# Optimization experiments

Hardware: AMD Instinct MI355X
Metric: run time of the kernel (lower is better)

## Reference

```python
import jax, jax.numpy as jnp
import numpy as np


def _gru(x, w_ih, w_hh, b_ih, b_hh, reverse=False):
    # PyTorch GRU cell math. x: (N, T, Din) -> (N, T, Hh)
    N, T, _ = x.shape
    Hh = w_hh.shape[1]
    xp = jnp.einsum('ntd,gd->ntg', x, w_ih) + b_ih  # (N, T, 3*Hh), input gates precomputed

    def step(h, xp_t):
        gh = h @ w_hh.T + b_hh
        ir, iz, inn = jnp.split(xp_t, 3, axis=-1)
        hr, hz, hn = jnp.split(gh, 3, axis=-1)
        r = jax.nn.sigmoid(ir + hr)
        z = jax.nn.sigmoid(iz + hz)
        n = jnp.tanh(inn + r * hn)
        h_new = (1.0 - z) * n + z * h
        return h_new, h_new

    h0 = jnp.zeros((N, Hh), x.dtype)
    _, ys = jax.lax.scan(step, h0, jnp.swapaxes(xp, 0, 1), reverse=reverse)
    return jnp.swapaxes(ys, 0, 1)


def _bigru(x, pf, pb):
    return jnp.concatenate([_gru(x, *pf), _gru(x, *pb, reverse=True)], axis=-1)


def _attn(out, w, b, ctx):
    # out: (N, T, H). tanh(Linear) -> context dot -> softmax -> weighted sum
    u = jnp.tanh(jnp.einsum('nth,gh->ntg', out, w) + b)
    a = jax.nn.softmax(u @ ctx, axis=-1)  # (N, T)
    return jnp.einsum('nt,nth->nh', a, out)


def setup_inputs() -> dict:
    key = jax.random.key(0)
    H, Hh = 512, 256
    S, B, Nsent = 2048, 16, 16
    L = S // Nsent
    ks = jax.random.split(key, 32)

    def p(k, shape):
        return jax.random.normal(k, shape, jnp.float32) * 0.05

    starts = jnp.arange(Nsent, dtype=jnp.int32) * L
    spans = jnp.stack([starts, starts + L], axis=-1)  # (Nsent, 2)
    spans = jnp.broadcast_to(spans, (B, Nsent, 2))

    inp = {
        'token_feats': jax.random.normal(ks[0], (S, B, H), jnp.float32),
        'sentence_spans': spans,
        # word BiGRU params (forward / backward directions)
        'w_wih_f': p(ks[1], (3 * Hh, H)), 'w_whh_f': p(ks[2], (3 * Hh, Hh)),
        'w_bih_f': p(ks[3], (3 * Hh,)), 'w_bhh_f': p(ks[4], (3 * Hh,)),
        'w_wih_b': p(ks[5], (3 * Hh, H)), 'w_whh_b': p(ks[6], (3 * Hh, Hh)),
        'w_bih_b': p(ks[7], (3 * Hh,)), 'w_bhh_b': p(ks[8], (3 * Hh,)),
        # sentence BiGRU params
        's_wih_f': p(ks[9], (3 * Hh, H)), 's_whh_f': p(ks[10], (3 * Hh, Hh)),
        's_bih_f': p(ks[11], (3 * Hh,)), 's_bhh_f': p(ks[12], (3 * Hh,)),
        's_wih_b': p(ks[13], (3 * Hh, H)), 's_whh_b': p(ks[14], (3 * Hh, Hh)),
        's_bih_b': p(ks[15], (3 * Hh,)), 's_bhh_b': p(ks[16], (3 * Hh,)),
        # attention params
        'w_attn_w': p(ks[17], (H, H)), 'w_attn_b': p(ks[18], (H,)),
        'w_ctx': jax.random.normal(ks[19], (H,), jnp.float32),
        's_attn_w': p(ks[20], (H, H)), 's_attn_b': p(ks[21], (H,)),
        's_ctx': jax.random.normal(ks[22], (H,), jnp.float32),
    }
    return inp


def reference(token_feats, sentence_spans,
              w_wih_f, w_whh_f, w_bih_f, w_bhh_f,
              w_wih_b, w_whh_b, w_bih_b, w_bhh_b,
              s_wih_f, s_whh_f, s_bih_f, s_bhh_f,
              s_wih_b, s_whh_b, s_bih_b, s_bhh_b,
              w_attn_w, w_attn_b, w_ctx,
              s_attn_w, s_attn_b, s_ctx):
    S, B, H = token_feats.shape
    Nsent = sentence_spans.shape[1]
    L = S // Nsent  # uniform spans: segment b,i = tokens [i*L, (i+1)*L)

    x = jnp.swapaxes(token_feats, 0, 1)  # (B, S, H)
    segs = x.reshape(B * Nsent, L, H)    # all sentences batched together

    # word-level BiGRU + word attention -> sentence vectors
    out_w = _bigru(segs, (w_wih_f, w_whh_f, w_bih_f, w_bhh_f),
                   (w_wih_b, w_whh_b, w_bih_b, w_bhh_b))  # (B*Nsent, L, H)
    sent_vecs = _attn(out_w, w_attn_w, w_attn_b, w_ctx).reshape(B, Nsent, H)

    # sentence-level BiGRU + sentence attention (no padding: all masks true)
    out_s = _bigru(sent_vecs, (s_wih_f, s_whh_f, s_bih_f, s_bhh_f),
                   (s_wih_b, s_whh_b, s_bih_b, s_bhh_b))  # (B, Nsent, H)
    Yh = _attn(out_s, s_attn_w, s_attn_b, s_ctx)  # (B, H)
    return Yh
```

## Files before the change

kernel.cpp:

```cpp
#include <hip/hip_runtime.h>
#include <stdint.h>


using uint32  = unsigned int;
using bf16x8  = __attribute__((ext_vector_type(8))) __bf16;
using floatx4 = __attribute__((ext_vector_type(4))) float;

__device__ __forceinline__ float b2f(unsigned short u) {
    union { uint32 i; float f; } v; v.i = ((uint32)u) << 16; return v.f;
}
__device__ __forceinline__ unsigned short f2b(float f) {
    union { float f; uint32 i; } v; v.f = f;
    uint32 r = v.i + 0x7fffu + ((v.i >> 16) & 1u);
    return (unsigned short)(r >> 16);
}
__device__ __forceinline__ float sigmoidf_(float x) { return 1.f / (1.f + __expf(-x)); }
__device__ __forceinline__ float tanhf_(float x) {
    x = fminf(15.f, fmaxf(-15.f, x));
    float e = __expf(2.f * x);
    return (e - 1.f) / (e + 1.f);
}

__device__ __forceinline__ void gl16(const unsigned short* g, unsigned short* l) {
    __builtin_amdgcn_global_load_lds(
        (const __attribute__((address_space(1))) uint32*)g,
        (__attribute__((address_space(3))) uint32*)l, 16, 0, 0);
}

__device__ __forceinline__ void bar_lgkm() {
    asm volatile("s_waitcnt lgkmcnt(0)");
    __builtin_amdgcn_sched_barrier(0);
    __builtin_amdgcn_s_barrier();
    __builtin_amdgcn_sched_barrier(0);
}

#define O_XPC     0L
#define O_OWHI    50331648L
#define O_OWLO    83886080L
#define O_STATE   117440512L
#define O_SCW     117964800L
#define O_W0HI    118095872L
#define O_W0LO    118882304L
#define O_W1HI    119668736L
#define O_W1LO    120455168L
#define O_WAHI    121241600L
#define O_WALO    121765888L
#define O_S0HI    122290176L
#define O_S0LO    123076608L
#define O_S1HI    123863040L
#define O_S1LO    124649472L
#define O_SAHI    125435904L
#define O_SALO    125960192L
#define O_HW0     126484480L
#define O_HW1     126877696L
#define O_HS0     127270912L
#define O_HS1     127664128L
#define O_SENTHI  128057344L
#define O_SENTLO  128319488L
#define O_XPS     128581632L
#define O_SSTATE  130154496L
#define O_OSHI    130187264L
#define O_OSLO    130449408L
#define O_SCS     130711552L
#define O_TKWH    130712576L
#define O_TKWL    164267008L

__global__ __launch_bounds__(256)
void cvt_hilo6(const float* __restrict__ s0, const float* __restrict__ s1,
               const float* __restrict__ s2, const float* __restrict__ s3,
               const float* __restrict__ s4, const float* __restrict__ s5,
               char* __restrict__ ws)
{
    const int b = blockIdx.x;
    const float* src; unsigned short *hi, *lo; int base;
    if (b < 192)      { src = s0; hi = (unsigned short*)(ws + O_W0HI); lo = (unsigned short*)(ws + O_W0LO); base = b; }
    else if (b < 384) { src = s1; hi = (unsigned short*)(ws + O_W1HI); lo = (unsigned short*)(ws + O_W1LO); base = b - 192; }
    else if (b < 576) { src = s2; hi = (unsigned short*)(ws + O_S0HI); lo = (unsigned short*)(ws + O_S0LO); base = b - 384; }
    else if (b < 768) { src = s3; hi = (unsigned short*)(ws + O_S1HI); lo = (unsigned short*)(ws + O_S1LO); base = b - 576; }
    else if (b < 896) { src = s4; hi = (unsigned short*)(ws + O_WAHI); lo = (unsigned short*)(ws + O_WALO); base = b - 768; }
    else              { src = s5; hi = (unsigned short*)(ws + O_SAHI); lo = (unsigned short*)(ws + O_SALO); base = b - 896; }
    const int idx = (base * 256 + threadIdx.x) * 8;
    float f[8];
    *reinterpret_cast<float4*>(&f[0]) = *reinterpret_cast<const float4*>(src + idx);
    *reinterpret_cast<float4*>(&f[4]) = *reinterpret_cast<const float4*>(src + idx + 4);
    unsigned short h[8], l[8];
    #pragma unroll
    for (int j = 0; j < 8; ++j) {
        h[j] = f2b(f[j]);
        l[j] = f2b(f[j] - b2f(h[j]));
    }
    *reinterpret_cast<uint4*>(hi + idx) = *reinterpret_cast<const uint4*>(h);
    *reinterpret_cast<uint4*>(lo + idx) = *reinterpret_cast<const uint4*>(l);
}

__global__ __launch_bounds__(256)
void cvt_b4(const float* __restrict__ s0, const float* __restrict__ s1,
            const float* __restrict__ s2, const float* __restrict__ s3,
            char* __restrict__ ws)
{
    const int b = blockIdx.x;
    const float* src; unsigned short* dst; int base;
    if (b < 96)       { src = s0; dst = (unsigned short*)(ws + O_HW0); base = b; }
    else if (b < 192) { src = s1; dst = (unsigned short*)(ws + O_HW1); base = b - 96; }
    else if (b < 288) { src = s2; dst = (unsigned short*)(ws + O_HS0); base = b - 192; }
    else              { src = s3; dst = (unsigned short*)(ws + O_HS1); base = b - 288; }
    const int idx = (base * 256 + threadIdx.x) * 8;
    float f[8];
    *reinterpret_cast<float4*>(&f[0]) = *reinterpret_cast<const float4*>(src + idx);
    *reinterpret_cast<float4*>(&f[4]) = *reinterpret_cast<const float4*>(src + idx + 4);
    unsigned short o[8];
    #pragma unroll
    for (int j = 0; j < 8; ++j) o[j] = f2b(f[j]);
    *reinterpret_cast<uint4*>(dst + idx) = *reinterpret_cast<const uint4*>(o);
}

__global__ __launch_bounds__(256)
void cvt_tokfull(const float* __restrict__ tok, unsigned short* __restrict__ whi,
                 unsigned short* __restrict__ wlo)
{
    const int u = blockIdx.x * 256 + threadIdx.x;
    const int h8 = u & 63;
    const int rest = u >> 6;
    const int t = rest & 127, seq = rest >> 7;
    const int sent = seq & 15, b = seq >> 4;
    const long src = ((long)(sent * 128 + t) * 16 + b) * 512 + h8 * 8;
    float f[8];
    *reinterpret_cast<float4*>(&f[0]) = *reinterpret_cast<const float4*>(tok + src);
    *reinterpret_cast<float4*>(&f[4]) = *reinterpret_cast<const float4*>(tok + src + 4);
    unsigned short h[8], l[8];
    #pragma unroll
    for (int j = 0; j < 8; ++j) {
        h[j] = f2b(f[j]);
        l[j] = f2b(f[j] - b2f(h[j]));
    }
    const long dst = (long)rest * 512 + h8 * 8;
    *reinterpret_cast<uint4*>(whi + dst) = *reinterpret_cast<const uint4*>(h);
    *reinterpret_cast<uint4*>(wlo + dst) = *reinterpret_cast<const uint4*>(l);
}

template<int AMODE>
__device__ __forceinline__ long amap(int m, int t0, int sgn) {
    if (AMODE == 1) {
        const int sq = m >> 5, tl = m & 31;
        return (long)(sq * 128 + t0 + sgn * tl) * 512;
    } else if (AMODE == 3) {
        const int n = m >> 4, tl = m & 15;
        return (long)(n * 16 + t0 + sgn * tl) * 512;
    }
    return (long)m * 512;
}

template<int AMODE, int OUT>
__global__ __launch_bounds__(512, 2)
void gemm_t(const unsigned short* __restrict__ Ahi, const unsigned short* __restrict__ Alo,
            const unsigned short* __restrict__ Wh0, const unsigned short* __restrict__ Wl0,
            const unsigned short* __restrict__ Wh1, const unsigned short* __restrict__ Wl1,
            const float* __restrict__ b0, const float* __restrict__ b1,
            float* __restrict__ C, int ldC, long c1off,
            float* __restrict__ score, const float* __restrict__ ctx,
            int t00, int t01, int nbyHalf)
{
    __shared__ __align__(16) unsigned short smem[2 * 32768];

    int bx = blockIdx.x, by = blockIdx.y;
    {
        const int nbx = gridDim.x, nby = gridDim.y;
        if ((nby & 7) == 0) {
            const int l = by * nbx + bx;
            const int xcd = l & 7;
            const int s = l >> 3;
            bx = s % nbx;
            by = xcd * (nby >> 3) + s / nbx;
        }
    }

    const int tid  = threadIdx.x;
    const int lane = tid & 63;
    const int wave = tid >> 6;
    const int wm = wave >> 2, wn = wave & 3;
    const int n_base = bx * 256;
    const int q = lane >> 4;
    const int r = lane & 15;

    const unsigned short* Whi = Wh0;
    const unsigned short* Wlo = Wl0;
    const float* bias = b0;
    float* Cb = C;
    int t0 = t00, sgn = 1, m_base;
    if (nbyHalf > 0 && by >= nbyHalf) {
        Whi = Wh1; Wlo = Wl1; bias = b1; Cb = C + c1off;
        t0 = t01; sgn = -1;
        m_base = (by - nbyHalf) * 256;
    } else {
        m_base = by * 256;
    }

    long aoff[2], woff[2];
    #pragma unroll
    for (int i = 0; i < 2; ++i) {
        const int s = tid + 512 * i;
        const int R = s >> 2, kg = s & 3;
        const int kq = (kg - (R >> 1)) & 3;
        aoff[i] = amap<AMODE>(m_base + R, t0, sgn) + kq * 8;
        woff[i] = (long)(n_base + R) * 512 + kq * 8;
    }

    floatx4 acc[8][4];
    #pragma unroll
    for (int mt = 0; mt < 8; ++mt)
        #pragma unroll
        for (int nt = 0; nt < 4; ++nt) acc[mt][nt] = (floatx4){0.f, 0.f, 0.f, 0.f};

    auto stage = [&](int ts) {
        const int k0 = ts * 32;
        unsigned short* B = smem + (ts & 1) * 32768;
        #pragma unroll
        for (int i = 0; i < 2; ++i) {
            const int ld = (tid + 512 * i) * 8;
            gl16(Ahi + aoff[i] + k0, B + ld);
            gl16(Alo + aoff[i] + k0, B + 8192 + ld);
            gl16(Whi + woff[i] + k0, B + 16384 + ld);
            gl16(Wlo + woff[i] + k0, B + 24576 + ld);
        }
    };

    stage(0);
    asm volatile("s_waitcnt vmcnt(0)");
    __builtin_amdgcn_sched_barrier(0);
    __builtin_amdgcn_s_barrier();
    __builtin_amdgcn_sched_barrier(0);

    for (int t = 0; t < 16; ++t) {
        if (t + 1 < 16) stage(t + 1);

        const unsigned short* B   = smem + (t & 1) * 32768;
        const unsigned short* BAl = B + 8192;
        const unsigned short* BW  = B + 16384;
        const unsigned short* BWl = B + 24576;

        bf16x8 wh[4], wl[4], ah[8], al[8];
        #pragma unroll
        for (int nt = 0; nt < 4; ++nt) {
            const int Rn = wn * 64 + nt * 16 + r;
            const int sn = Rn * 4 + ((q + (Rn >> 1)) & 3);
            wh[nt] = *reinterpret_cast<const bf16x8*>(BW  + sn * 8);
            wl[nt] = *reinterpret_cast<const bf16x8*>(BWl + sn * 8);
        }
        #pragma unroll
        for (int mt = 0; mt < 8; ++mt) {
            const int R = wm * 128 + mt * 16 + r;
            const int s = R * 4 + ((q + (R >> 1)) & 3);
            ah[mt] = *reinterpret_cast<const bf16x8*>(B   + s * 8);
            al[mt] = *reinterpret_cast<const bf16x8*>(BAl + s * 8);
        }
        asm volatile("s_waitcnt lgkmcnt(0)");
        __builtin_amdgcn_sched_barrier(0);

        #pragma unroll
        for (int mt = 0; mt < 8; ++mt)
            #pragma unroll
            for (int nt = 0; nt < 4; ++nt) {
                acc[mt][nt] = __builtin_amdgcn_mfma_f32_16x16x32_bf16(ah[mt], wh[nt], acc[mt][nt], 0, 0, 0);
                acc[mt][nt] = __builtin_amdgcn_mfma_f32_16x16x32_bf16(ah[mt], wl[nt], acc[mt][nt], 0, 0, 0);
                acc[mt][nt] = __builtin_amdgcn_mfma_f32_16x16x32_bf16(al[mt], wh[nt], acc[mt][nt], 0, 0, 0);
            }

        __builtin_amdgcn_sched_barrier(0);
        asm volatile("s_waitcnt vmcnt(0)");
        __builtin_amdgcn_sched_barrier(0);
        __builtin_amdgcn_s_barrier();
        __builtin_amdgcn_sched_barrier(0);
    }

    if (OUT == 0) {
        #pragma unroll
        for (int nt = 0; nt < 4; ++nt) {
            const int n = n_base + wn * 64 + nt * 16 + r;
            const float bs = bias[n];
            #pragma unroll
            for (int mt = 0; mt < 8; ++mt) {
                const int m = m_base + wm * 128 + mt * 16 + q * 4;
                #pragma unroll
                for (int e = 0; e < 4; ++e)
                    Cb[(long)(m + e) * ldC + n] = acc[mt][nt][e] + bs;
            }
        }
    } else {
        #pragma unroll
        for (int mt = 0; mt < 8; ++mt) {
            float p[4] = {0.f, 0.f, 0.f, 0.f};
            #pragma unroll
            for (int nt = 0; nt < 4; ++nt) {
                const int n = n_base + wn * 64 + nt * 16 + r;
                const float cx = ctx[n];
                const float bs = bias[n];
                #pragma unroll
                for (int e = 0; e < 4; ++e)
                    p[e] += cx * tanhf_(acc[mt][nt][e] + bs);
            }
            #pragma unroll
            for (int mk = 1; mk < 16; mk <<= 1) {
                #pragma unroll
                for (int e = 0; e < 4; ++e) p[e] += __shfl_xor(p[e], mk, 64);
            }
            if (r == 0) {
                const int m = m_base + wm * 128 + mt * 16 + q * 4;
                #pragma unroll
                for (int e = 0; e < 4; ++e)
                    atomicAdd(&score[m + e], p[e]);
            }
        }
    }
}

template<int AMODE, int OUT>
__global__ __launch_bounds__(256)
void gemm_d(const unsigned short* __restrict__ Ahi, const unsigned short* __restrict__ Alo,
            const unsigned short* __restrict__ Wh0, const unsigned short* __restrict__ Wl0,
            const unsigned short* __restrict__ Wh1, const unsigned short* __restrict__ Wl1,
            const float* __restrict__ b0, const float* __restrict__ b1,
            float* __restrict__ C, int ldC, long c1off,
            float* __restrict__ score, const float* __restrict__ ctx,
            int t00, int t01, int nbyHalf)
{
    __shared__ __align__(16) unsigned short smem[2 * 16384];

    int bx = blockIdx.x, by = blockIdx.y;
    {
        const int nbx = gridDim.x, nby = gridDim.y;
        if ((nby & 7) == 0) {
            const int l = by * nbx + bx;
            const int xcd = l & 7;
            const int s = l >> 3;
            bx = s % nbx;
            by = xcd * (nby >> 3) + s / nbx;
        }
    }

    const int tid  = threadIdx.x;
    const int lane = tid & 63;
    const int wave = tid >> 6;
    const int wm = wave >> 1, wn = wave & 1;
    const int n_base = bx * 128;
    const int q = lane >> 4;
    const int r = lane & 15;

    const unsigned short* Whi = Wh0;
    const unsigned short* Wlo = Wl0;
    const float* bias = b0;
    float* Cb = C;
    int t0 = t00, sgn = 1, m_base;
    if (nbyHalf > 0 && by >= nbyHalf) {
        Whi = Wh1; Wlo = Wl1; bias = b1; Cb = C + c1off;
        t0 = t01; sgn = -1;
        m_base = (by - nbyHalf) * 128;
    } else {
        m_base = by * 128;
    }

    long aoff[2], woff[2];
    #pragma unroll
    for (int i = 0; i < 2; ++i) {
        const int s = tid + 256 * i;
        const int R = s >> 2, kg = s & 3;
        const int kq = (kg - (R >> 1)) & 3;
        aoff[i] = amap<AMODE>(m_base + R, t0, sgn) + kq * 8;
        woff[i] = (long)(n_base + R) * 512 + kq * 8;
    }

    floatx4 acc[4][4];
    #pragma unroll
    for (int mt = 0; mt < 4; ++mt)
        #pragma unroll
        for (int nt = 0; nt < 4; ++nt) acc[mt][nt] = (floatx4){0.f, 0.f, 0.f, 0.f};

    auto stage = [&](int ts) {
        const int k0 = ts * 32;
        unsigned short* B = smem + (ts & 1) * 16384;
        #pragma unroll
        for (int i = 0; i < 2; ++i) {
            const int ld = (tid + 256 * i) * 8;
            gl16(Ahi + aoff[i] + k0, B + ld);
            gl16(Alo + aoff[i] + k0, B + 4096 + ld);
            gl16(Whi + woff[i] + k0, B + 8192 + ld);
            gl16(Wlo + woff[i] + k0, B + 12288 + ld);
        }
    };

    stage(0);
    for (int t = 0; t < 16; ++t) {
        stage(t + 1 < 16 ? t + 1 : 15);
        asm volatile("s_waitcnt vmcnt(8)\n\ts_barrier" ::: "memory");

        const unsigned short* B = smem + (t & 1) * 16384;
        bf16x8 ah[4], al[4];
        #pragma unroll
        for (int mt = 0; mt < 4; ++mt) {
            const int R = wm * 64 + mt * 16 + r;
            const int s = R * 4 + ((q + (R >> 1)) & 3);
            ah[mt] = *reinterpret_cast<const bf16x8*>(B + s * 8);
            al[mt] = *reinterpret_cast<const bf16x8*>(B + 4096 + s * 8);
        }
        #pragma unroll
        for (int nt = 0; nt < 4; ++nt) {
            const int Rn = wn * 64 + nt * 16 + r;
            const int sn = Rn * 4 + ((q + (Rn >> 1)) & 3);
            bf16x8 wh = *reinterpret_cast<const bf16x8*>(B + 8192 + sn * 8);
            bf16x8 wl = *reinterpret_cast<const bf16x8*>(B + 12288 + sn * 8);
            #pragma unroll
            for (int mt = 0; mt < 4; ++mt) {
                acc[mt][nt] = __builtin_amdgcn_mfma_f32_16x16x32_bf16(ah[mt], wh, acc[mt][nt], 0, 0, 0);
                acc[mt][nt] = __builtin_amdgcn_mfma_f32_16x16x32_bf16(ah[mt], wl, acc[mt][nt], 0, 0, 0);
                acc[mt][nt] = __builtin_amdgcn_mfma_f32_16x16x32_bf16(al[mt], wh, acc[mt][nt], 0, 0, 0);
            }
        }
        asm volatile("s_waitcnt lgkmcnt(0)\n\ts_barrier" ::: "memory");
    }
    asm volatile("s_waitcnt vmcnt(0)" ::: "memory");

    if (OUT == 0) {
        #pragma unroll
        for (int nt = 0; nt < 4; ++nt) {
            const int n = n_base + wn * 64 + nt * 16 + r;
            const float bs = bias[n];
            #pragma unroll
            for (int mt = 0; mt < 4; ++mt) {
                const int m = m_base + wm * 64 + mt * 16 + q * 4;
                #pragma unroll
                for (int e = 0; e < 4; ++e)
                    Cb[(long)(m + e) * ldC + n] = acc[mt][nt][e] + bs;
            }
        }
    } else {
        #pragma unroll
        for (int mt = 0; mt < 4; ++mt) {
            float p[4] = {0.f, 0.f, 0.f, 0.f};
            #pragma unroll
            for (int nt = 0; nt < 4; ++nt) {
                const int n = n_base + wn * 64 + nt * 16 + r;
                const float cx = ctx[n];
                const float bs = bias[n];
                #pragma unroll
                for (int e = 0; e < 4; ++e)
                    p[e] += cx * tanhf_(acc[mt][nt][e] + bs);
            }
            #pragma unroll
            for (int mk = 1; mk < 16; mk <<= 1) {
                #pragma unroll
                for (int e = 0; e < 4; ++e) p[e] += __shfl_xor(p[e], mk, 64);
            }
            if (r == 0) {
                const int m = m_base + wm * 64 + mt * 16 + q * 4;
                #pragma unroll
                for (int e = 0; e < 4; ++e)
                    atomicAdd(&score[m + e], p[e]);
            }
        }
    }
}

__global__ __launch_bounds__(512, 2)
void gru2(const float* __restrict__ xp,
          const unsigned short* __restrict__ Wf,
          const unsigned short* __restrict__ Wb,
          const float* __restrict__ bhf, const float* __restrict__ bhb,
          float* __restrict__ state,
          unsigned short* __restrict__ ohi, unsigned short* __restrict__ olo,
          int steps, int t0f, int t0b, int groups, int Tout)
{
    __shared__ float preS[8][6][16][4];
    __shared__ unsigned short Bf[2][4096];

    const int tid  = threadIdx.x;
    const int lane = tid & 63;
    const int w    = tid >> 6;
    const int dir  = blockIdx.x / groups;
    const int g    = blockIdx.x % groups;
    const int nseq = groups * 2;
    const unsigned short* W = dir ? Wb : Wf;
    const float* bh = dir ? bhb : bhf;
    const int t0  = dir ? t0b : t0f;
    const int sgn = dir ? -1 : 1;

    const int s  = lane & 1;
    const int lr = lane >> 1;
    const int u  = w * 32 + lr;

    const float bhr = bh[u], bhz = bh[u + 256], bhn = bh[u + 512];

    bf16x8 wf[6][8];
    {
        const int rl = lane & 15;
        const int kf = (lane >> 4) * 8;
        #pragma unroll
        for (int mt = 0; mt < 6; ++mt) {
            const int R = (mt >> 1) * 256 + w * 32 + (mt & 1) * 16 + rl;
            #pragma unroll
            for (int kk = 0; kk < 8; ++kk)
                wf[mt][kk] = *reinterpret_cast<const bf16x8*>(
                    W + (long)R * 256 + kk * 32 + kf);
        }
    }

    #pragma unroll
    for (int i = 0; i < 8; ++i)
        reinterpret_cast<uint32*>(Bf)[tid * 8 + i] = 0;

    float h = state[((long)dir * nseq + g * 2 + s) * 256 + u];
    const int bposHi = (w * 64 + (lr >> 3) * 16 + s) * 8 + (lr & 7);
    const int bposLo = (w * 64 + (lr >> 3) * 16 + 2 + s) * 8 + (lr & 7);
    {
        const unsigned short hb = f2b(h);
        Bf[0][bposHi] = hb;
        Bf[0][bposLo] = f2b(h - b2f(hb));
    }
    bar_lgkm();

    const float* xbase = xp + (long)dir * nseq * steps * 768
                       + (long)(g * 2 + s) * steps * 768;

    float xr = xbase[u], xz = xbase[256 + u], xn = xbase[512 + u];

    const int c  = lane & 15;
    const int q  = lane >> 4;
    const int rit  = lr & 15;
    const int hsel = lr >> 4;

    for (int st = 0; st < steps; ++st) {
        const int t = t0 + sgn * st;
        const int cur = st & 1;

        const int sn2 = (st + 1 < steps) ? st + 1 : st;
        const float* xb = xbase + (long)sn2 * 768;
        const float nxr = xb[u];
        const float nxz = xb[256 + u];
        const float nxn = xb[512 + u];

        floatx4 acc[6];
        #pragma unroll
        for (int mt = 0; mt < 6; ++mt) acc[mt] = (floatx4){0.f, 0.f, 0.f, 0.f};
        #pragma unroll
        for (int kk = 0; kk < 8; ++kk) {
            bf16x8 bv = *reinterpret_cast<const bf16x8*>(&Bf[cur][(kk * 64 + lane) * 8]);
            #pragma unroll
            for (int mt = 0; mt < 6; ++mt)
                acc[mt] = __builtin_amdgcn_mfma_f32_16x16x32_bf16(wf[mt][kk], bv, acc[mt], 0, 0, 0);
        }

        if (c < 4) {
            #pragma unroll
            for (int mt = 0; mt < 6; ++mt)
                #pragma unroll
                for (int e = 0; e < 4; ++e)
                    preS[w][mt][q * 4 + e][c] = acc[mt][e];
        }
        asm volatile("s_waitcnt lgkmcnt(0)");
        __builtin_amdgcn_sched_barrier(0);

        {
            const float4 fr = *reinterpret_cast<const float4*>(&preS[w][0 + hsel][rit][0]);
            const float4 fz = *reinterpret_cast<const float4*>(&preS[w][2 + hsel][rit][0]);
            const float4 fn = *reinterpret_cast<const float4*>(&preS[w][4 + hsel][rit][0]);
            const float pr = (s ? fr.y : fr.x) + (s ? fr.w : fr.z);
            const float pz = (s ? fz.y : fz.x) + (s ? fz.w : fz.z);
            const float pn = (s ? fn.y : fn.x) + (s ? fn.w : fn.z);
            const float rg = sigmoidf_(xr + pr + bhr);
            const float zg = sigmoidf_(xz + pz + bhz);
            const float nn = tanhf_(xn + rg * (pn + bhn));
            h = (1.f - zg) * nn + zg * h;
            const unsigned short hb = f2b(h);
            const unsigned short lb = f2b(h - b2f(hb));
            Bf[cur ^ 1][bposHi] = hb;
            Bf[cur ^ 1][bposLo] = lb;
            const long orow = ((long)(g * 2 + s) * Tout + t) * 512 + dir * 256 + u;
            ohi[orow] = hb;
            olo[orow] = lb;
        }
        xr = nxr; xz = nxz; xn = nxn;
        bar_lgkm();
    }

    state[((long)dir * nseq + g * 2 + s) * 256 + u] = h;
}

template<int MODE, int T>
__global__ __launch_bounds__(256)
void attn_wsum(const float* __restrict__ score,
               const unsigned short* __restrict__ fhi,
               const unsigned short* __restrict__ flo,
               void* __restrict__ o1, void* __restrict__ o2)
{
    const int n = blockIdx.x;
    const int tid = threadIdx.x;
    __shared__ float a[T];
    __shared__ float e[T];
    if (tid < T) a[tid] = score[n * T + tid];
    __syncthreads();
    float mx = -1e30f;
    #pragma unroll
    for (int t = 0; t < T; ++t) mx = fmaxf(mx, a[t]);
    if (tid < T) e[tid] = __expf(a[tid] - mx);
    __syncthreads();
    float sm = 0.f;
    #pragma unroll
    for (int t = 0; t < T; ++t) sm += e[t];
    const float inv = 1.f / sm;
    float acc0 = 0.f, acc1 = 0.f;
    #pragma unroll 8
    for (int t = 0; t < T; ++t) {
        const float w = e[t] * inv;
        const long base = ((long)n * T + t) * 512;
        acc0 += w * (b2f(fhi[base + tid])       + b2f(flo[base + tid]));
        acc1 += w * (b2f(fhi[base + tid + 256]) + b2f(flo[base + tid + 256]));
    }
    if (MODE == 1) {
        float* o = (float*)o1;
        o[n * 512 + tid] = acc0;
        o[n * 512 + tid + 256] = acc1;
    } else {
        unsigned short* oh = (unsigned short*)o1;
        unsigned short* ol = (unsigned short*)o2;
        const unsigned short h0 = f2b(acc0), h1 = f2b(acc1);
        oh[n * 512 + tid]       = h0;  ol[n * 512 + tid]       = f2b(acc0 - b2f(h0));
        oh[n * 512 + tid + 256] = h1;  ol[n * 512 + tid + 256] = f2b(acc1 - b2f(h1));
    }
}

extern "C" void kernel_launch(void* const* d_in, const int* in_sizes, int n_in,
                              void* d_out, int out_size, void* d_ws, size_t ws_size,
                              hipStream_t stream) {
    const float* tok      = (const float*)d_in[0];
    const float* w_wih_f  = (const float*)d_in[2];
    const float* w_whh_f  = (const float*)d_in[3];
    const float* w_bih_f  = (const float*)d_in[4];
    const float* w_bhh_f  = (const float*)d_in[5];
    const float* w_wih_b  = (const float*)d_in[6];
    const float* w_whh_b  = (const float*)d_in[7];
    const float* w_bih_b  = (const float*)d_in[8];
    const float* w_bhh_b  = (const float*)d_in[9];
    const float* s_wih_f  = (const float*)d_in[10];
    const float* s_whh_f  = (const float*)d_in[11];
    const float* s_bih_f  = (const float*)d_in[12];
    const float* s_bhh_f  = (const float*)d_in[13];
    const float* s_wih_b  = (const float*)d_in[14];
    const float* s_whh_b  = (const float*)d_in[15];
    const float* s_bih_b  = (const float*)d_in[16];
    const float* s_bhh_b  = (const float*)d_in[17];
    const float* w_attn_b = (const float*)d_in[19];
    const float* w_ctx    = (const float*)d_in[20];
    const float* s_attn_b = (const float*)d_in[22];
    const float* s_ctx    = (const float*)d_in[23];

    char* ws = (char*)d_ws;
    float*          xpc   = (float*)(ws + O_XPC);
    unsigned short* owhi  = (unsigned short*)(ws + O_OWHI);
    unsigned short* owlo  = (unsigned short*)(ws + O_OWLO);
    float*          state = (float*)(ws + O_STATE);
    float*          score_w = (float*)(ws + O_SCW);
    unsigned short* W0HI  = (unsigned short*)(ws + O_W0HI);
    unsigned short* W0LO  = (unsigned short*)(ws + O_W0LO);
    unsigned short* W1HI  = (unsigned short*)(ws + O_W1HI);
    unsigned short* W1LO  = (unsigned short*)(ws + O_W1LO);
    unsigned short* WAHI  = (unsigned short*)(ws + O_WAHI);
    unsigned short* WALO  = (unsigned short*)(ws + O_WALO);
    unsigned short* S0HI  = (unsigned short*)(ws + O_S0HI);
    unsigned short* S0LO  = (unsigned short*)(ws + O_S0LO);
    unsigned short* S1HI  = (unsigned short*)(ws + O_S1HI);
    unsigned short* S1LO  = (unsigned short*)(ws + O_S1LO);
    unsigned short* SAHI  = (unsigned short*)(ws + O_SAHI);
    unsigned short* SALO  = (unsigned short*)(ws + O_SALO);
    unsigned short* HW0   = (unsigned short*)(ws + O_HW0);
    unsigned short* HW1   = (unsigned short*)(ws + O_HW1);
    unsigned short* HS0   = (unsigned short*)(ws + O_HS0);
    unsigned short* HS1   = (unsigned short*)(ws + O_HS1);
    unsigned short* senthi = (unsigned short*)(ws + O_SENTHI);
    unsigned short* sentlo = (unsigned short*)(ws + O_SENTLO);
    float*          xp_s  = (float*)(ws + O_XPS);
    float*          sstate = (float*)(ws + O_SSTATE);
    unsigned short* oshi  = (unsigned short*)(ws + O_OSHI);
    unsigned short* oslo  = (unsigned short*)(ws + O_OSLO);
    float*          score_s = (float*)(ws + O_SCS);
    unsigned short* tkwh  = (unsigned short*)(ws + O_TKWH);
    unsigned short* tkwl  = (unsigned short*)(ws + O_TKWL);

    const dim3 blk(256);

    hipMemsetAsync(ws + O_STATE,  0, 524288, stream);
    hipMemsetAsync(ws + O_SSTATE, 0, 32768, stream);
    hipMemsetAsync(ws + O_SCW,    0, 131072, stream);
    hipMemsetAsync(ws + O_SCS,    0, 1024, stream);

    cvt_hilo6<<<dim3(1024), blk, 0, stream>>>(w_wih_f, w_wih_b, s_wih_f, s_wih_b,
                                              (const float*)d_in[18], (const float*)d_in[21], ws);
    cvt_b4<<<dim3(384), blk, 0, stream>>>(w_whh_f, w_whh_b, s_whh_f, s_whh_b, ws);
    cvt_tokfull<<<dim3(8192), blk, 0, stream>>>(tok, tkwh, tkwl);

    const long XDW = 256L * 32 * 768;
    for (int c = 0; c < 4; ++c) {
        gemm_t<1, 0><<<dim3(3, 64), dim3(512), 0, stream>>>(
            tkwh, tkwl, W0HI, W0LO, W1HI, W1LO, w_bih_f, w_bih_b,
            xpc, 768, XDW, nullptr, nullptr, 32 * c, 127 - 32 * c, 32);
        gru2<<<dim3(256), dim3(512), 0, stream>>>(
            xpc, HW0, HW1, w_bhh_f, w_bhh_b, state, owhi, owlo,
            32, 32 * c, 127 - 32 * c, 128, 128);
    }

    gemm_t<2, 1><<<dim3(2, 128), dim3(512), 0, stream>>>(
        owhi, owlo, WAHI, WALO, WAHI, WALO, w_attn_b, w_attn_b,
        nullptr, 0, 0, score_w, w_ctx, 0, 0, 0);
    attn_wsum<0, 128><<<dim3(256), blk, 0, stream>>>(score_w, owhi, owlo, senthi, sentlo);

    const long XDS = 16L * 16 * 768;
    gemm_d<3, 0><<<dim3(6, 4), blk, 0, stream>>>(
        senthi, sentlo, S0HI, S0LO, S1HI, S1LO, s_bih_f, s_bih_b,
        xp_s, 768, XDS, nullptr, nullptr, 0, 15, 2);

    gru2<<<dim3(16), dim3(512), 0, stream>>>(
        xp_s, HS0, HS1, s_bhh_f, s_bhh_b, sstate, oshi, oslo,
        16, 0, 15, 8, 16);

    gemm_d<2, 1><<<dim3(4, 2), blk, 0, stream>>>(
        oshi, oslo, SAHI, SALO, SAHI, SALO, s_attn_b, s_attn_b,
        nullptr, 0, 0, score_s, s_ctx, 0, 0, 0);
    attn_wsum<1, 16><<<dim3(16), blk, 0, stream>>>(score_s, oshi, oslo, d_out, nullptr);
}
```

Before: 678.1 us.

## Repartition GRU recurrence to 4 waves with 64 hidden units per wave

Rewrites the recurrent GRU kernel to use 256 threads (4 waves) instead of 512. Each wave now holds 12 MFMA row tiles of the recurrent weights in registers, and each lane computes both sequences for one hidden unit. The preS scratch layout changes so accumulator rows are written as float4. The goal is to cut per-step barrier cost and cross-wave synchronisation in the latency-bound sequential loop. The cost is that the 96 bf16x8 weight fragments per lane roughly double register pressure and risk spills, and each wave issues twice as many MFMAs per step.

```diff
diff --git a/kernel.cpp b/kernel.cpp
--- a/kernel.cpp
+++ b/kernel.cpp
@@ -459,8 +459,8 @@
     }
 }
 
-__global__ __launch_bounds__(512, 2)
-void gru2(const float* __restrict__ xp,
+__global__ __launch_bounds__(256, 1)
+void gru4(const float* __restrict__ xp,
           const unsigned short* __restrict__ Wf,
           const unsigned short* __restrict__ Wb,
           const float* __restrict__ bhf, const float* __restrict__ bhb,
@@ -468,7 +468,7 @@
           unsigned short* __restrict__ ohi, unsigned short* __restrict__ olo,
           int steps, int t0f, int t0b, int groups, int Tout)
 {
-    __shared__ float preS[8][6][16][4];
+    __shared__ float preS[4][12][4][16];
     __shared__ unsigned short Bf[2][4096];
 
     const int tid  = threadIdx.x;
@@ -482,19 +482,16 @@
     const int t0  = dir ? t0b : t0f;
     const int sgn = dir ? -1 : 1;
 
-    const int s  = lane & 1;
-    const int lr = lane >> 1;
-    const int u  = w * 32 + lr;
-
+    const int u = w * 64 + lane;
     const float bhr = bh[u], bhz = bh[u + 256], bhn = bh[u + 512];
 
-    bf16x8 wf[6][8];
+    bf16x8 wf[12][8];
     {
         const int rl = lane & 15;
         const int kf = (lane >> 4) * 8;
         #pragma unroll
-        for (int mt = 0; mt < 6; ++mt) {
-            const int R = (mt >> 1) * 256 + w * 32 + (mt & 1) * 16 + rl;
+        for (int mt = 0; mt < 12; ++mt) {
+            const int R = (mt >> 2) * 256 + w * 64 + (mt & 3) * 16 + rl;
             #pragma unroll
             for (int kk = 0; kk < 8; ++kk)
                 wf[mt][kk] = *reinterpret_cast<const bf16x8*>(
@@ -503,84 +500,98 @@
     }
 
     #pragma unroll
-    for (int i = 0; i < 8; ++i)
-        reinterpret_cast<uint32*>(Bf)[tid * 8 + i] = 0;
-
-    float h = state[((long)dir * nseq + g * 2 + s) * 256 + u];
-    const int bposHi = (w * 64 + (lr >> 3) * 16 + s) * 8 + (lr & 7);
-    const int bposLo = (w * 64 + (lr >> 3) * 16 + 2 + s) * 8 + (lr & 7);
+    for (int i = 0; i < 16; ++i)
+        reinterpret_cast<uint32*>(Bf)[tid * 16 + i] = 0;
+
+    float h0 = state[((long)dir * nseq + g * 2 + 0) * 256 + u];
+    float h1 = state[((long)dir * nseq + g * 2 + 1) * 256 + u];
+    const int bbase = ((u >> 5) * 64 + ((u >> 3) & 3) * 16) * 8 + (u & 7);
     {
-        const unsigned short hb = f2b(h);
-        Bf[0][bposHi] = hb;
-        Bf[0][bposLo] = f2b(h - b2f(hb));
+        const unsigned short hb0 = f2b(h0), hb1 = f2b(h1);
+        Bf[0][bbase]      = hb0;
+        Bf[0][bbase + 8]  = hb1;
+        Bf[0][bbase + 16] = f2b(h0 - b2f(hb0));
+        Bf[0][bbase + 24] = f2b(h1 - b2f(hb1));
     }
     bar_lgkm();
 
-    const float* xbase = xp + (long)dir * nseq * steps * 768
-                       + (long)(g * 2 + s) * steps * 768;
-
-    float xr = xbase[u], xz = xbase[256 + u], xn = xbase[512 + u];
-
-    const int c  = lane & 15;
-    const int q  = lane >> 4;
-    const int rit  = lr & 15;
-    const int hsel = lr >> 4;
+    const float* xb0 = xp + ((long)dir * nseq + g * 2 + 0) * steps * 768;
+    const float* xb1 = xp + ((long)dir * nseq + g * 2 + 1) * steps * 768;
+
+    float xr0 = xb0[u], xz0 = xb0[256 + u], xn0 = xb0[512 + u];
+    float xr1 = xb1[u], xz1 = xb1[256 + u], xn1 = xb1[512 + u];
+
+    const int c = lane & 15;
+    const int q = lane >> 4;
+    const int sub = lane >> 4;
+    const int rit = lane & 15;
 
     for (int st = 0; st < steps; ++st) {
         const int t = t0 + sgn * st;
         const int cur = st & 1;
 
         const int sn2 = (st + 1 < steps) ? st + 1 : st;
-        const float* xb = xbase + (long)sn2 * 768;
-        const float nxr = xb[u];
-        const float nxz = xb[256 + u];
-        const float nxn = xb[512 + u];
-
-        floatx4 acc[6];
-        #pragma unroll
-        for (int mt = 0; mt < 6; ++mt) acc[mt] = (floatx4){0.f, 0.f, 0.f, 0.f};
+        const float* xa = xb0 + (long)sn2 * 768;
+        const float* xc = xb1 + (long)sn2 * 768;
+        const float nxr0 = xa[u], nxz0 = xa[256 + u], nxn0 = xa[512 + u];
+        const float nxr1 = xc[u], nxz1 = xc[256 + u], nxn1 = xc[512 + u];
+
+        floatx4 acc[12];
+        #pragma unroll
+        for (int mt = 0; mt < 12; ++mt) acc[mt] = (floatx4){0.f, 0.f, 0.f, 0.f};
         #pragma unroll
         for (int kk = 0; kk < 8; ++kk) {
             bf16x8 bv = *reinterpret_cast<const bf16x8*>(&Bf[cur][(kk * 64 + lane) * 8]);
             #pragma unroll
-            for (int mt = 0; mt < 6; ++mt)
+            for (int mt = 0; mt < 12; ++mt)
                 acc[mt] = __builtin_amdgcn_mfma_f32_16x16x32_bf16(wf[mt][kk], bv, acc[mt], 0, 0, 0);
         }
 
         if (c < 4) {
             #pragma unroll
-            for (int mt = 0; mt < 6; ++mt)
-                #pragma unroll
-                for (int e = 0; e < 4; ++e)
-                    preS[w][mt][q * 4 + e][c] = acc[mt][e];
+            for (int mt = 0; mt < 12; ++mt)
+                *reinterpret_cast<float4*>(&preS[w][mt][c][q * 4]) =
+                    *reinterpret_cast<const float4*>(&acc[mt]);
         }
         asm volatile("s_waitcnt lgkmcnt(0)");
         __builtin_amdgcn_sched_barrier(0);
 
         {
-            const float4 fr = *reinterpret_cast<const float4*>(&preS[w][0 + hsel][rit][0]);
-            const float4 fz = *reinterpret_cast<const float4*>(&preS[w][2 + hsel][rit][0]);
-            const float4 fn = *reinterpret_cast<const float4*>(&preS[w][4 + hsel][rit][0]);
-            const float pr = (s ? fr.y : fr.x) + (s ? fr.w : fr.z);
-            const float pz = (s ? fz.y : fz.x) + (s ? fz.w : fz.z);
-            const float pn = (s ? fn.y : fn.x) + (s ? fn.w : fn.z);
-            const float rg = sigmoidf_(xr + pr + bhr);
-            const float zg = sigmoidf_(xz + pz + bhz);
-            const float nn = tanhf_(xn + rg * (pn + bhn));
-            h = (1.f - zg) * nn + zg * h;
-            const unsigned short hb = f2b(h);
-            const unsigned short lb = f2b(h - b2f(hb));
-            Bf[cur ^ 1][bposHi] = hb;
-            Bf[cur ^ 1][bposLo] = lb;
-            const long orow = ((long)(g * 2 + s) * Tout + t) * 512 + dir * 256 + u;
-            ohi[orow] = hb;
-            olo[orow] = lb;
-        }
-        xr = nxr; xz = nxz; xn = nxn;
+            const float pr0 = preS[w][0 + sub][0][rit] + preS[w][0 + sub][2][rit];
+            const float pr1 = preS[w][0 + sub][1][rit] + preS[w][0 + sub][3][rit];
+            const float pz0 = preS[w][4 + sub][0][rit] + preS[w][4 + sub][2][rit];
+            const float pz1 = preS[w][4 + sub][1][rit] + preS[w][4 + sub][3][rit];
+            const float pn0 = preS[w][8 + sub][0][rit] + preS[w][8 + sub][2][rit];
+            const float pn1 = preS[w][8 + sub][1][rit] + preS[w][8 + sub][3][rit];
+
+            const float rg0 = sigmoidf_(xr0 + pr0 + bhr);
+            const float zg0 = sigmoidf_(xz0 + pz0 + bhz);
+            const float nn0 = tanhf_(xn0 + rg0 * (pn0 + bhn));
+            h0 = (1.f - zg0) * nn0 + zg0 * h0;
+            const float rg1 = sigmoidf_(xr1 + pr1 + bhr);
+            const float zg1 = sigmoidf_(xz1 + pz1 + bhz);
+            const float nn1 = tanhf_(xn1 + rg1 * (pn1 + bhn));
+            h1 = (1.f - zg1) * nn1 + zg1 * h1;
+
+            const unsigned short hb0 = f2b(h0), hb1 = f2b(h1);
+            const unsigned short lb0 = f2b(h0 - b2f(hb0));
+            const unsigned short lb1 = f2b(h1 - b2f(hb1));
+            Bf[cur ^ 1][bbase]      = hb0;
+            Bf[cur ^ 1][bbase + 8]  = hb1;
+            Bf[cur ^ 1][bbase + 16] = lb0;
+            Bf[cur ^ 1][bbase + 24] = lb1;
+            const long o0 = ((long)(g * 2 + 0) * Tout + t) * 512 + dir * 256 + u;
+            const long o1 = ((long)(g * 2 + 1) * Tout + t) * 512 + dir * 256 + u;
+            ohi[o0] = hb0;  olo[o0] = lb0;
+            ohi[o1] = hb1;  olo[o1] = lb1;
+        }
+        xr0 = nxr0; xz0 = nxz0; xn0 = nxn0;
+        xr1 = nxr1; xz1 = nxz1; xn1 = nxn1;
         bar_lgkm();
     }
 
-    state[((long)dir * nseq + g * 2 + s) * 256 + u] = h;
+    state[((long)dir * nseq + g * 2 + 0) * 256 + u] = h0;
+    state[((long)dir * nseq + g * 2 + 1) * 256 + u] = h1;
 }
 
 template<int MODE, int T>
@@ -700,7 +711,7 @@
         gemm_t<1, 0><<<dim3(3, 64), dim3(512), 0, stream>>>(
             tkwh, tkwl, W0HI, W0LO, W1HI, W1LO, w_bih_f, w_bih_b,
             xpc, 768, XDW, nullptr, nullptr, 32 * c, 127 - 32 * c, 32);
-        gru2<<<dim3(256), dim3(512), 0, stream>>>(
+        gru4<<<dim3(256), dim3(256), 0, stream>>>(
             xpc, HW0, HW1, w_bhh_f, w_bhh_b, state, owhi, owlo,
             32, 32 * c, 127 - 32 * c, 128, 128);
     }
@@ -715,7 +726,7 @@
         senthi, sentlo, S0HI, S0LO, S1HI, S1LO, s_bih_f, s_bih_b,
         xp_s, 768, XDS, nullptr, nullptr, 0, 15, 2);
 
-    gru2<<<dim3(16), dim3(512), 0, stream>>>(
+    gru4<<<dim3(16), dim3(256), 0, stream>>>(
         xp_s, HS0, HS1, s_bhh_f, s_bhh_b, sstate, oshi, oslo,
         16, 0, 15, 8, 16);
 
```

Result: slower. 759.2 us (+12.0%).
